# Kernel tuning notes

Hardware: AMD Instinct MI355X
Metric: run time of the kernel (lower is better)

## Reference

```python
import jax, jax.numpy as jnp
import numpy as np

P = 7    # output_size (7,7)
SR = 2   # sampling_ratio per bin (torchvision roi_align samples per bin)


def _roi_avg_pool(feature_map, rois):
    """Fused roi_align(output_size=PxP) + adaptive_avg_pool2d(1,1).

    Since every bin averages SR*SR equally-weighted samples and the global
    average pool then averages the P*P bins, the result equals the mean over
    all P*SR x P*SR bilinear samples -- the 7x7 grid is never materialized.
    """
    B, C, H, W = feature_map.shape
    bidx = rois[:, 0].astype(jnp.int32)                       # [N]
    # get_anns: fp32 math, stored into an fp16 tensor (replicate the rounding).
    # NOTE (faithful to source): x coords are scaled by H (shape[2]) and y by W.
    f16 = lambda v: v.astype(jnp.float16).astype(jnp.float32)
    x1 = f16((rois[:, 2] - 0.5 * rois[:, 4]) * H)
    y1 = f16((rois[:, 3] - 0.5 * rois[:, 5]) * W)
    x2 = f16((rois[:, 2] + 0.5 * rois[:, 4]) * H)
    y2 = f16((rois[:, 3] + 0.5 * rois[:, 5]) * W)

    # torchvision roi_align, spatial_scale=1, aligned=False
    roi_w = jnp.maximum(x2 - x1, 1.0)
    roi_h = jnp.maximum(y2 - y1, 1.0)
    # sample offsets: bin pw plus (ix+0.5)/SR within the bin, in units of bin size
    offs = (jnp.arange(P, dtype=jnp.float32)[:, None]
            + (jnp.arange(SR, dtype=jnp.float32)[None, :] + 0.5) / SR).reshape(-1)  # [P*SR]
    xs = x1[:, None] + offs[None, :] * (roi_w / P)[:, None]   # [N,S] along width
    ys = y1[:, None] + offs[None, :] * (roi_h / P)[:, None]   # [N,S] along height

    valid = (((ys > -1.0) & (ys < H))[:, :, None]
             & ((xs > -1.0) & (xs < W))[:, None, :])          # [N,S,S]
    yc = jnp.clip(ys, 0.0, H - 1.0)
    xc = jnp.clip(xs, 0.0, W - 1.0)
    y0 = jnp.floor(yc).astype(jnp.int32)
    x0 = jnp.floor(xc).astype(jnp.int32)
    y1i = jnp.minimum(y0 + 1, H - 1)
    x1i = jnp.minimum(x0 + 1, W - 1)
    ly = yc - y0
    lx = xc - x0
    hy = 1.0 - ly
    hx = 1.0 - lx

    feat_t = jnp.transpose(feature_map, (0, 2, 3, 1))         # [B,H,W,C]

    def gather(yy, xx):  # yy,xx: [N,S] -> [N,S,S,C]
        return feat_t[bidx[:, None, None], yy[:, :, None], xx[:, None, :]]

    w = lambda a, b: (a[:, :, None] * b[:, None, :])[..., None]
    val = (w(hy, hx) * gather(y0, x0) + w(hy, lx) * gather(y0, x1i)
           + w(ly, hx) * gather(y1i, x0) + w(ly, lx) * gather(y1i, x1i))
    val = jnp.where(valid[..., None], val, 0.0)
    return val.mean(axis=(1, 2))                              # [N,C]


def setup_inputs() -> dict:
    key = jax.random.key(0)
    k1, k2, k3, k4 = jax.random.split(key, 4)
    B, C, H, W, N = 4, 256, 128, 128, 512
    feature_map = jax.random.normal(k1, (B, C, H, W), dtype=jnp.float32)
    # sorted batch indices so the original per-batch regrouping keeps ROI order
    bidx = jnp.sort(jax.random.randint(k2, (N,), 0, B)).astype(jnp.float32)
    cls = jax.random.randint(k3, (N,), 0, 20).astype(jnp.float32)
    kc, kw = jax.random.split(k4)
    cxcy = jax.random.uniform(kc, (N, 2), minval=0.2, maxval=0.8, dtype=jnp.float32)
    wh = jax.random.uniform(kw, (N, 2), minval=0.05, maxval=0.4, dtype=jnp.float32)
    rois = jnp.concatenate([bidx[:, None], cls[:, None], cxcy, wh], axis=1)  # [N,6]
    return {"feature_map": feature_map, "rois": rois}


def reference(feature_map, rois):
    roi_feats = _roi_avg_pool(feature_map, rois)   # [N, C] (original returns len-N list of [1,C])
    gt = rois[:, 1]                                # class labels
    return roi_feats, gt
```

## Files before the change

kernel.cpp:

```cpp
#include <hip/hip_runtime.h>
#include <hip/hip_fp16.h>
#include <hip/hip_bf16.h>

#define PP 7
#define SR 2
#define HH 128
#define WW 128
#define CC 256
#define PLANE (HH * WW)
#define MAXB 8
#define SLOT_BYTES 32768
#define WY_BASE (8 * SLOT_BYTES)
#define TAB_OFF (2 * WY_BASE)

typedef unsigned int uint;
typedef short bf16x8 __attribute__((ext_vector_type(8)));
typedef float f32x16 __attribute__((ext_vector_type(16)));

typedef const __attribute__((address_space(1))) void g_void;
typedef __attribute__((address_space(3))) void l_void;

__device__ __forceinline__ void gload_lds16(const void* g, void* lds_base) {
  __builtin_amdgcn_global_load_lds((g_void*)g, (l_void*)lds_base, 16, 0, 0);
}

__device__ __forceinline__ uint pkbf(float a, float b) {
  __hip_bfloat16 ha = __float2bfloat16(a), hb = __float2bfloat16(b);
  return (uint)*(unsigned short*)&ha | ((uint)*(unsigned short*)&hb << 16);
}

__global__ __launch_bounds__(64) void setup_kernel(
    const float* __restrict__ rois, unsigned char* wsb, int N, int B) {
  __shared__ int c[MAXB];
  const int t = threadIdx.x;
  if (t < MAXB) c[t] = 0;
  __syncthreads();
  for (int j = t; j < N; j += 64) atomicAdd(&c[(int)rois[j * 6]], 1);
  __syncthreads();
  if (t == 0) {
    int* tab = (int*)(wsb + TAB_OFF);
    int s = 0, tb = 0;
    for (int i = 0; i < B; ++i) {
      tab[i] = s; tab[24 + i] = c[i];
      const int tc = (c[i] + 127) >> 7;
      tab[8 + i] = tc; tab[16 + i] = tb;
      s += c[i]; tb += tc;
    }
  }
}

__global__ __launch_bounds__(64) void roi_meta_kernel(
    const float* __restrict__ rois, unsigned char* wsb,
    float* __restrict__ out, int N) {
  const int roi = blockIdx.x;
  const int lane = threadIdx.x;

  __shared__ float WXs[WW], WYs[HH];
  WXs[lane] = 0.f; WXs[lane + 64] = 0.f;
  WYs[lane] = 0.f; WYs[lane + 64] = 0.f;
  __syncthreads();

  const float bf = rois[roi * 6 + 0];
  const float cx = rois[roi * 6 + 2];
  const float cy = rois[roi * 6 + 3];
  const float w_ = rois[roi * 6 + 4];
  const float h_ = rois[roi * 6 + 5];

  const float x1 = __half2float(__float2half(
      __fmul_rn(__fsub_rn(cx, __fmul_rn(0.5f, w_)), 128.0f)));
  const float y1 = __half2float(__float2half(
      __fmul_rn(__fsub_rn(cy, __fmul_rn(0.5f, h_)), 128.0f)));
  const float x2 = __half2float(__float2half(
      __fmul_rn(__fadd_rn(cx, __fmul_rn(0.5f, w_)), 128.0f)));
  const float y2 = __half2float(__float2half(
      __fmul_rn(__fadd_rn(cy, __fmul_rn(0.5f, h_)), 128.0f)));

  const float sx = fmaxf(__fsub_rn(x2, x1), 1.0f) / 7.0f;
  const float sy = fmaxf(__fsub_rn(y2, y1), 1.0f) / 7.0f;

  if (lane < 2 * PP * SR) {
    const int isX = lane >= PP * SR;
    const int i = lane - isX * PP * SR;
    const float off = (float)(i >> 1) + ((float)(i & 1) + 0.5f) * 0.5f;
    const float pos = __fadd_rn(isX ? x1 : y1, __fmul_rn(off, isX ? sx : sy));
    if (pos > -1.0f && pos < 128.0f) {
      const float pc = fminf(fmaxf(pos, 0.0f), 127.0f);
      const int p0 = (int)floorf(pc);
      const int p1 = min(p0 + 1, 127);
      const float l = pc - (float)p0;
      float* Warr = isX ? WXs : WYs;
      atomicAdd(&Warr[p0], 1.0f - l);
      atomicAdd(&Warr[p1], l);
    }
  }
  __syncthreads();

  const int* tab = (const int*)(wsb + TAB_OFF);
  const int img = (int)bf;
  const int rl = roi - tab[img];
  const int slot = tab[16 + img] + (rl >> 7);
  const int col = rl & 127;

  const int sw = ((((lane >> 2) ^ (col & 7)) << 4) | ((lane & 3) << 2));
  *(uint*)(wsb + (size_t)slot * SLOT_BYTES + col * 256 + sw) =
      pkbf(WXs[2 * lane], WXs[2 * lane + 1]);
  __hip_bfloat16 h0 = __float2bfloat16(WYs[lane]);
  __hip_bfloat16 h1 = __float2bfloat16(WYs[lane + 64]);
  unsigned char* wyb = wsb + WY_BASE + (size_t)slot * SLOT_BYTES + col * 2;
  *(unsigned short*)(wyb + lane * 256) = *(unsigned short*)&h0;
  *(unsigned short*)(wyb + (lane + 64) * 256) = *(unsigned short*)&h1;

  if (lane == 0) out[(size_t)N * CC + roi] = rois[roi * 6 + 1];
}

__global__ __launch_bounds__(256, 2) void roi_gemm_kernel(
    const float* __restrict__ fm, const unsigned char* __restrict__ wsb,
    float* __restrict__ out, int N) {
  const int bid = blockIdx.x;
  const int ch = bid & (CC - 1);
  const int img = bid >> 8;
  const int t = threadIdx.x, wave = t >> 6, lane = t & 63;

  const int* tab = (const int*)(wsb + TAB_OFF);
  const int tcnt = tab[8 + img];
  if (tcnt == 0) return;
  const int istart = tab[img], Rimg = tab[24 + img], tbase = tab[16 + img];

  __shared__ unsigned char A[32768];
  __shared__ unsigned char BXl[32768];
  __shared__ float partial[4][128];

  auto stage_bx = [&](int ti) {
    const unsigned char* BXg = wsb + (size_t)(tbase + ti) * SLOT_BYTES;
    #pragma unroll
    for (int k2 = 0; k2 < 8; ++k2)
      gload_lds16(BXg + k2 * 4096 + wave * 1024 + (lane << 4),
                  BXl + k2 * 4096 + wave * 1024);
  };

  stage_bx(0);

  const float* pb = fm + ((size_t)img * CC + ch) * PLANE;
  float4 u[16];
  #pragma unroll
  for (int k = 0; k < 8; ++k) {
    const int cid = k * 256 + t;
    u[2 * k]     = *(const float4*)(pb + (size_t)cid * 8);
    u[2 * k + 1] = *(const float4*)(pb + (size_t)cid * 8 + 4);
  }
  __builtin_amdgcn_sched_barrier(0);
  #pragma unroll
  for (int k = 0; k < 8; ++k) {
    const int cid = k * 256 + t;
    const int row = cid >> 4, x8 = cid & 15;
    const int boff = (row << 8) | ((x8 ^ (row & 7)) << 4);
    uint4 P;
    P.x = pkbf(u[2 * k].x, u[2 * k].y); P.y = pkbf(u[2 * k].z, u[2 * k].w);
    P.z = pkbf(u[2 * k + 1].x, u[2 * k + 1].y); P.w = pkbf(u[2 * k + 1].z, u[2 * k + 1].w);
    *(uint4*)(A + boff) = P;
  }
  asm volatile("s_waitcnt vmcnt(0)" ::: "memory");
  __syncthreads();

  const int m0 = wave * 32;
  const int arow = m0 + (lane & 31);
  const int ar7 = arow & 7;
  const unsigned char* Arow = A + (arow << 8);
  const int ahalf = lane >> 5;
  const int r7 = lane & 7;

  for (int ti = 0; ti < tcnt; ++ti) {
    if (ti > 0) {
      stage_bx(ti);
      asm volatile("s_waitcnt vmcnt(0)" ::: "memory");
      __syncthreads();
    }
    const unsigned char* BY = wsb + WY_BASE + (size_t)(tbase + ti) * SLOT_BYTES;

    f32x16 ac0 = {}, ac1 = {}, ac2 = {}, ac3 = {};

    auto ldA = [&](int ks) -> bf16x8 {
      const int idx = (ahalf + 2 * ks) ^ ar7;
      return *(const bf16x8*)(Arow + (idx << 4));
    };
    auto ldB = [&](int ks, int ni) -> bf16x8 {
      const int c = (2 * ks + ahalf) ^ r7;
      return *(const bf16x8*)(BXl + (((lane & 31) + 32 * ni) << 8) + (c << 4));
    };

    bf16x8 a = ldA(0);
    bf16x8 b0 = ldB(0, 0), b1 = ldB(0, 1), b2 = ldB(0, 2), b3 = ldB(0, 3);
    #pragma unroll
    for (int ks = 0; ks < 8; ++ks) {
      bf16x8 an{}, bn0{}, bn1{}, bn2{}, bn3{};
      if (ks < 7) {
        an = ldA(ks + 1);
        bn0 = ldB(ks + 1, 0); bn1 = ldB(ks + 1, 1);
        bn2 = ldB(ks + 1, 2); bn3 = ldB(ks + 1, 3);
      }
      ac0 = __builtin_amdgcn_mfma_f32_32x32x16_bf16(a, b0, ac0, 0, 0, 0);
      ac1 = __builtin_amdgcn_mfma_f32_32x32x16_bf16(a, b1, ac1, 0, 0, 0);
      ac2 = __builtin_amdgcn_mfma_f32_32x32x16_bf16(a, b2, ac2, 0, 0, 0);
      ac3 = __builtin_amdgcn_mfma_f32_32x32x16_bf16(a, b3, ac3, 0, 0, 0);
      a = an; b0 = bn0; b1 = bn1; b2 = bn2; b3 = bn3;
    }

    #pragma unroll
    for (int ni = 0; ni < 4; ++ni) {
      const f32x16 acc = ni == 0 ? ac0 : ni == 1 ? ac1 : ni == 2 ? ac2 : ac3;
      float p = 0.f;
      #pragma unroll
      for (int j = 0; j < 16; ++j) {
        const int y = m0 + (j & 3) + 8 * (j >> 2) + 4 * ahalf;
        const unsigned short wy =
            *(const unsigned short*)(BY + y * 256 + (ni * 32 + (lane & 31)) * 2);
        p = fmaf(__uint_as_float((uint)wy << 16), acc[j], p);
      }
      p += __shfl_xor(p, 32, 64);
      if (lane < 32) partial[wave][ni * 32 + lane] = p;
    }
    __syncthreads();
    if (t < 128) {
      const int rl = ti * 128 + t;
      if (rl < Rimg) {
        const float s = partial[0][t] + partial[1][t] + partial[2][t] + partial[3][t];
        out[(size_t)(istart + rl) * CC + ch] = s * (1.0f / 196.0f);
      }
    }
    __syncthreads();
  }
}

extern "C" void kernel_launch(void* const* d_in, const int* in_sizes, int n_in,
                              void* d_out, int out_size, void* d_ws, size_t ws_size,
                              hipStream_t stream) {
  const float* fm   = (const float*)d_in[0];
  const float* rois = (const float*)d_in[1];
  float* out = (float*)d_out;
  unsigned char* wsb = (unsigned char*)d_ws;
  const int N = in_sizes[1] / 6;
  const int B = in_sizes[0] / (CC * PLANE);
  setup_kernel<<<1, 64, 0, stream>>>(rois, wsb, N, B);
  roi_meta_kernel<<<N, 64, 0, stream>>>(rois, wsb, out, N);
  roi_gemm_kernel<<<B * CC, 256, 0, stream>>>(fm, wsb, out, N);
}
```

Baseline: 32.06 us.

## Drop setup kernel via in-kernel binary search; relayout WY weights for vector loads

```diff
diff --git a/kernel.cpp b/kernel.cpp
--- a/kernel.cpp
+++ b/kernel.cpp
@@ -8,10 +8,8 @@
 #define WW 128
 #define CC 256
 #define PLANE (HH * WW)
-#define MAXB 8
 #define SLOT_BYTES 32768
 #define WY_BASE (8 * SLOT_BYTES)
-#define TAB_OFF (2 * WY_BASE)
 
 typedef unsigned int uint;
 typedef short bf16x8 __attribute__((ext_vector_type(8)));
@@ -29,35 +27,27 @@
   return (uint)*(unsigned short*)&ha | ((uint)*(unsigned short*)&hb << 16);
 }
 
-__global__ __launch_bounds__(64) void setup_kernel(
-    const float* __restrict__ rois, unsigned char* wsb, int N, int B) {
-  __shared__ int c[MAXB];
-  const int t = threadIdx.x;
-  if (t < MAXB) c[t] = 0;
-  __syncthreads();
-  for (int j = t; j < N; j += 64) atomicAdd(&c[(int)rois[j * 6]], 1);
-  __syncthreads();
-  if (t == 0) {
-    int* tab = (int*)(wsb + TAB_OFF);
-    int s = 0, tb = 0;
-    for (int i = 0; i < B; ++i) {
-      tab[i] = s; tab[24 + i] = c[i];
-      const int tc = (c[i] + 127) >> 7;
-      tab[8 + i] = tc; tab[16 + i] = tb;
-      s += c[i]; tb += tc;
-    }
-  }
+__device__ __forceinline__ int lb_img(const float* rois, int N, float v) {
+  int lo = 0, hi = N;
+  while (lo < hi) {
+    const int mid = (lo + hi) >> 1;
+    if (rois[mid * 6] < v) lo = mid + 1; else hi = mid;
+  }
+  return lo;
 }
 
 __global__ __launch_bounds__(64) void roi_meta_kernel(
     const float* __restrict__ rois, unsigned char* wsb,
-    float* __restrict__ out, int N) {
+    float* __restrict__ out, int N, int B) {
   const int roi = blockIdx.x;
   const int lane = threadIdx.x;
 
   __shared__ float WXs[WW], WYs[HH];
   WXs[lane] = 0.f; WXs[lane + 64] = 0.f;
   WYs[lane] = 0.f; WYs[lane + 64] = 0.f;
+
+  int lbv = 0;
+  if (lane <= B) lbv = lb_img(rois, N, (float)lane);
   __syncthreads();
 
   const float bf = rois[roi * 6 + 0];
@@ -95,36 +85,54 @@
   }
   __syncthreads();
 
-  const int* tab = (const int*)(wsb + TAB_OFF);
   const int img = (int)bf;
-  const int rl = roi - tab[img];
-  const int slot = tab[16 + img] + (rl >> 7);
+  const int myStart = __shfl(lbv, img, 64);
+  int tb = 0;
+  for (int i = 0; i < img; ++i)
+    tb += (__shfl(lbv, i + 1, 64) - __shfl(lbv, i, 64) + 127) >> 7;
+  const int rl = roi - myStart;
+  const int slot = tb + (rl >> 7);
   const int col = rl & 127;
+  const int ni = col >> 5, c31 = col & 31;
 
   const int sw = ((((lane >> 2) ^ (col & 7)) << 4) | ((lane & 3) << 2));
   *(uint*)(wsb + (size_t)slot * SLOT_BYTES + col * 256 + sw) =
       pkbf(WXs[2 * lane], WXs[2 * lane + 1]);
-  __hip_bfloat16 h0 = __float2bfloat16(WYs[lane]);
-  __hip_bfloat16 h1 = __float2bfloat16(WYs[lane + 64]);
-  unsigned char* wyb = wsb + WY_BASE + (size_t)slot * SLOT_BYTES + col * 2;
-  *(unsigned short*)(wyb + lane * 256) = *(unsigned short*)&h0;
-  *(unsigned short*)(wyb + (lane + 64) * 256) = *(unsigned short*)&h1;
+
+  unsigned char* wyb = wsb + WY_BASE + (size_t)slot * SLOT_BYTES;
+  #pragma unroll
+  for (int h = 0; h < 2; ++h) {
+    const int y = lane + 64 * h;
+    const int mtile = y >> 5, y5 = y & 31;
+    const int ahalf = (y5 >> 2) & 1;
+    const int j = (y5 & 3) | ((y5 >> 3) << 2);
+    const int ln = c31 | (ahalf << 5);
+    __hip_bfloat16 hv = __float2bfloat16(WYs[y]);
+    *(unsigned short*)(wyb + ((((mtile << 2) | ni) << 6 | ln) << 5) + (j << 1)) =
+        *(unsigned short*)&hv;
+  }
 
   if (lane == 0) out[(size_t)N * CC + roi] = rois[roi * 6 + 1];
 }
 
 __global__ __launch_bounds__(256, 2) void roi_gemm_kernel(
-    const float* __restrict__ fm, const unsigned char* __restrict__ wsb,
-    float* __restrict__ out, int N) {
+    const float* __restrict__ fm, const float* __restrict__ rois,
+    const unsigned char* __restrict__ wsb, float* __restrict__ out,
+    int N, int B) {
   const int bid = blockIdx.x;
   const int ch = bid & (CC - 1);
   const int img = bid >> 8;
   const int t = threadIdx.x, wave = t >> 6, lane = t & 63;
 
-  const int* tab = (const int*)(wsb + TAB_OFF);
-  const int tcnt = tab[8 + img];
-  if (tcnt == 0) return;
-  const int istart = tab[img], Rimg = tab[24 + img], tbase = tab[16 + img];
+  int lbv = 0;
+  if (lane <= B) lbv = lb_img(rois, N, (float)lane);
+  const int istart = __shfl(lbv, img, 64);
+  const int cnt = __shfl(lbv, img + 1, 64) - istart;
+  if (cnt == 0) return;
+  int tbase = 0;
+  for (int i = 0; i < img; ++i)
+    tbase += (__shfl(lbv, i + 1, 64) - __shfl(lbv, i, 64) + 127) >> 7;
+  const int tcnt = (cnt + 127) >> 7;
 
   __shared__ unsigned char A[32768];
   __shared__ unsigned char BXl[32768];
@@ -175,7 +183,7 @@
       asm volatile("s_waitcnt vmcnt(0)" ::: "memory");
       __syncthreads();
     }
-    const unsigned char* BY = wsb + WY_BASE + (size_t)(tbase + ti) * SLOT_BYTES;
+    const unsigned char* BYc = wsb + WY_BASE + (size_t)(tbase + ti) * SLOT_BYTES;
 
     f32x16 ac0 = {}, ac1 = {}, ac2 = {}, ac3 = {};
 
@@ -208,21 +216,34 @@
     #pragma unroll
     for (int ni = 0; ni < 4; ++ni) {
       const f32x16 acc = ni == 0 ? ac0 : ni == 1 ? ac1 : ni == 2 ? ac2 : ac3;
+      const uint* wp = (const uint*)(
+          BYc + ((((wave << 2) | ni) << 6 | lane) << 5));
+      const uint4 wlo = *(const uint4*)wp;
+      const uint4 whi = *(const uint4*)(wp + 4);
       float p = 0.f;
-      #pragma unroll
-      for (int j = 0; j < 16; ++j) {
-        const int y = m0 + (j & 3) + 8 * (j >> 2) + 4 * ahalf;
-        const unsigned short wy =
-            *(const unsigned short*)(BY + y * 256 + (ni * 32 + (lane & 31)) * 2);
-        p = fmaf(__uint_as_float((uint)wy << 16), acc[j], p);
-      }
+      p = fmaf(__uint_as_float(wlo.x << 16),         acc[0], p);
+      p = fmaf(__uint_as_float(wlo.x & 0xffff0000u), acc[1], p);
+      p = fmaf(__uint_as_float(wlo.y << 16),         acc[2], p);
+      p = fmaf(__uint_as_float(wlo.y & 0xffff0000u), acc[3], p);
+      p = fmaf(__uint_as_float(wlo.z << 16),         acc[4], p);
+      p = fmaf(__uint_as_float(wlo.z & 0xffff0000u), acc[5], p);
+      p = fmaf(__uint_as_float(wlo.w << 16),         acc[6], p);
+      p = fmaf(__uint_as_float(wlo.w & 0xffff0000u), acc[7], p);
+      p = fmaf(__uint_as_float(whi.x << 16),         acc[8], p);
+      p = fmaf(__uint_as_float(whi.x & 0xffff0000u), acc[9], p);
+      p = fmaf(__uint_as_float(whi.y << 16),         acc[10], p);
+      p = fmaf(__uint_as_float(whi.y & 0xffff0000u), acc[11], p);
+      p = fmaf(__uint_as_float(whi.z << 16),         acc[12], p);
+      p = fmaf(__uint_as_float(whi.z & 0xffff0000u), acc[13], p);
+      p = fmaf(__uint_as_float(whi.w << 16),         acc[14], p);
+      p = fmaf(__uint_as_float(whi.w & 0xffff0000u), acc[15], p);
       p += __shfl_xor(p, 32, 64);
       if (lane < 32) partial[wave][ni * 32 + lane] = p;
     }
     __syncthreads();
     if (t < 128) {
       const int rl = ti * 128 + t;
-      if (rl < Rimg) {
+      if (rl < cnt) {
         const float s = partial[0][t] + partial[1][t] + partial[2][t] + partial[3][t];
         out[(size_t)(istart + rl) * CC + ch] = s * (1.0f / 196.0f);
       }
@@ -240,7 +261,6 @@
   unsigned char* wsb = (unsigned char*)d_ws;
   const int N = in_sizes[1] / 6;
   const int B = in_sizes[0] / (CC * PLANE);
-  setup_kernel<<<1, 64, 0, stream>>>(rois, wsb, N, B);
-  roi_meta_kernel<<<N, 64, 0, stream>>>(rois, wsb, out, N);
-  roi_gemm_kernel<<<B * CC, 256, 0, stream>>>(fm, wsb, out, N);
-}
+  roi_meta_kernel<<<N, 64, 0, stream>>>(rois, wsb, out, N, B);
+  roi_gemm_kernel<<<B * CC, 256, 0, stream>>>(fm, rois, wsb, out, N, B);
+}
```

Result: slower. 33.89 us (+5.7%).
